# Performance work log

Hardware: AMD Instinct MI355X
Metric: run time of the kernel (lower is better)

## Reference

```python
import jax, jax.numpy as jnp
from jax import lax
import numpy as np

HID = 64      # lstm hidden / gat in-dim
HEADS = 4
DH = HID // HEADS  # 16 per-head dim
OUT = 3       # horizon


def setup_inputs() -> dict:
    key = jax.random.key(0)
    ks = jax.random.split(key, 18)
    B, T, N = 8, 12, 1500
    p = lambda k, shape: jax.random.normal(k, shape, jnp.float32) * 0.1
    return {
        "x": jax.random.normal(ks[0], (B, T, N), jnp.float32),
        "adj": jax.random.randint(ks[1], (N, N), 0, 2, jnp.int32),
        "lstm_Wih0": p(ks[2], (4 * HID, 1)),
        "lstm_Whh0": p(ks[3], (4 * HID, HID)),
        "lstm_bih0": p(ks[4], (4 * HID,)),
        "lstm_bhh0": p(ks[5], (4 * HID,)),
        "lstm_Wih1": p(ks[6], (4 * HID, HID)),
        "lstm_Whh1": p(ks[7], (4 * HID, HID)),
        "lstm_bih1": p(ks[8], (4 * HID,)),
        "lstm_bhh1": p(ks[9], (4 * HID,)),
        "gat0_W": p(ks[10], (HID, HID)),
        "gat0_asrc": p(ks[11], (HEADS, DH)),
        "gat0_adst": p(ks[12], (HEADS, DH)),
        "gat1_W": p(ks[13], (HID, HID)),
        "gat1_asrc": p(ks[14], (HEADS, DH)),
        "gat1_adst": p(ks[15], (HEADS, DH)),
        "out_W": p(ks[16], (OUT, HID)),
        "out_b": p(ks[17], (OUT,)),
    }


def _lstm_layer(seq, Wih, Whh, bih, bhh):
    # seq: (T, BN, in) -> (T, BN, H). PyTorch gate order i,f,g,o.
    BN = seq.shape[1]
    H = Whh.shape[1]

    def step(carry, xt):
        h, c = carry
        g = xt @ Wih.T + h @ Whh.T + bih + bhh
        i, f, gg, o = jnp.split(g, 4, axis=-1)
        c = jax.nn.sigmoid(f) * c + jax.nn.sigmoid(i) * jnp.tanh(gg)
        h = jax.nn.sigmoid(o) * jnp.tanh(c)
        return (h, c), h

    zero = jnp.zeros((BN, H), seq.dtype)
    _, hs = lax.scan(step, (zero, zero), seq)
    return hs


def _gat(h_in, W, asrc, adst, mask):
    # h_in: (B,N,HID); mask: (1,N,N,1) bool
    B, N, _ = h_in.shape
    Hn, D = asrc.shape
    hp = (h_in @ W.T).reshape(B, N, Hn, D)           # (B,N,H,D)
    e_src = jnp.einsum('bnhd,hd->bnh', hp, asrc)
    e_dst = jnp.einsum('bnhd,hd->bnh', hp, adst)
    e = e_src[:, :, None, :] + e_dst[:, None, :, :]   # (B,i,j,H)
    e = jnp.where(e > 0, e, 0.2 * e)                  # LeakyReLU(0.2)
    e = jnp.where(mask, e, -jnp.inf)
    alpha = jax.nn.softmax(e, axis=2)                 # softmax over neighbors j
    ho = jnp.einsum('bijh,bjhd->bihd', alpha, hp)
    return ho.reshape(B, N, Hn * D)


def reference(x, adj, lstm_Wih0, lstm_Whh0, lstm_bih0, lstm_bhh0,
              lstm_Wih1, lstm_Whh1, lstm_bih1, lstm_bhh1,
              gat0_W, gat0_asrc, gat0_adst, gat1_W, gat1_asrc, gat1_adst,
              out_W, out_b):
    B, T, N = x.shape
    # (B,T,N) -> (B*N, T, 1) -> time-major (T, B*N, 1)
    xf = jnp.transpose(x, (0, 2, 1)).reshape(B * N, T, 1)
    seq = jnp.transpose(xf, (1, 0, 2))
    hs = _lstm_layer(seq, lstm_Wih0, lstm_Whh0, lstm_bih0, lstm_bhh0)
    hs = _lstm_layer(hs, lstm_Wih1, lstm_Whh1, lstm_bih1, lstm_bhh1)
    h = hs[-1].reshape(B, N, HID)                     # last-step hidden of top layer
    mask = (adj > 0)[None, :, :, None]
    h = jax.nn.relu(_gat(h, gat0_W, gat0_asrc, gat0_adst, mask))
    h = jax.nn.relu(_gat(h, gat1_W, gat1_asrc, gat1_adst, mask))
    out = h @ out_W.T + out_b                         # (B,N,OUT)
    return jnp.transpose(out, (0, 2, 1))              # (B,OUT,N)
```

## Files before the change

### kernel.cpp

```cpp
#include <hip/hip_runtime.h>
#include <hip/hip_bf16.h>


#define BN 12000
#define NNODE 1500
#define NB 8
#define TT 12
#define NPAD 1536
#define LOG2E 1.44269504f

typedef __bf16 bf16x8 __attribute__((ext_vector_type(8)));
typedef __bf16 bf16x4 __attribute__((ext_vector_type(4)));
typedef float  f32x4  __attribute__((ext_vector_type(4)));

__device__ __forceinline__ float rcpf(float v) { return __builtin_amdgcn_rcpf(v); }
__device__ __forceinline__ float exp2f_(float v) { return __builtin_amdgcn_exp2f(v); }
__device__ __forceinline__ float sigf(float v) { return rcpf(1.f + __expf(-v)); }
__device__ __forceinline__ float tanhf_(float v) {
    return fmaf(2.f, rcpf(1.f + __expf(-2.f * v)), -1.f);
}

__device__ __forceinline__ bf16x8 ldcvt(const float* __restrict__ p) {
    f32x4 a = *(const f32x4*)p;
    f32x4 b = *(const f32x4*)(p + 4);
    bf16x8 r;
    #pragma unroll
    for (int i = 0; i < 4; ++i) { r[i] = (__bf16)a[i]; r[4 + i] = (__bf16)b[i]; }
    return r;
}

__global__ __launch_bounds__(512, 1) void lstm_mask(
    const float* __restrict__ x,
    const float* __restrict__ Wih0, const float* __restrict__ Whh0,
    const float* __restrict__ bih0, const float* __restrict__ bhh0,
    const float* __restrict__ Wih1, const float* __restrict__ Whh1,
    const float* __restrict__ bih1, const float* __restrict__ bhh1,
    const int* __restrict__ adj, unsigned int* __restrict__ mask,
    float* __restrict__ hfin)
{
    if (blockIdx.x >= 750) {
        int wid  = (blockIdx.x - 750) * 8 + (threadIdx.x >> 6);
        int lane = threadIdx.x & 63;
        #pragma unroll 4
        for (int u = 0; u < 16; ++u) {
            int task = wid * 16 + u;
            int i = task / 24, ch = task - i * 24;
            int j = ch * 64 + lane;
            int a = (i < NNODE && j < NNODE) ? adj[i * NNODE + j] : 0;
            unsigned long long m = __ballot(a > 0);
            if (lane == 0 && i < 1504) *(unsigned long long*)&mask[i * 48 + ch * 2] = m;
        }
        return;
    }

    __shared__ __align__(16) __bf16 h0s[16 * 72];
    __shared__ __align__(16) __bf16 h1s[16 * 72];
    __shared__ __align__(16) float  xls[TT * 16];

    int tid  = threadIdx.x;
    int w    = __builtin_amdgcn_readfirstlane(tid >> 6);
    int lane = tid & 63;
    int l15  = lane & 15;
    int qd   = lane >> 4;
    bool lo  = l15 < 8;
    int dloc = l15 & 7;
    int d    = 8 * w + dloc;

    for (int e = tid; e < (16 * 72) / 2; e += 512) ((unsigned int*)h1s)[e] = 0u;
    if (tid < TT * 16) {
        int t = tid >> 4, m = tid & 15;
        int s = blockIdx.x * 16 + m;
        int bb = s / NNODE, nn = s - bb * NNODE;
        xls[tid] = x[bb * (TT * NNODE) + t * NNODE + nn];
    }

    int gA = (lo ? 0 : 64) + d;
    int gB = (lo ? 128 : 192) + d;
    bf16x8 B0A[2], B0B[2], B1A[4], B1B[4];
    #pragma unroll
    for (int kt = 0; kt < 2; ++kt) {
        B0A[kt] = ldcvt(&Whh0[gA * 64 + 32 * kt + 8 * qd]);
        B0B[kt] = ldcvt(&Whh0[gB * 64 + 32 * kt + 8 * qd]);
        B1A[kt] = ldcvt(&Wih1[gA * 64 + 32 * kt + 8 * qd]);
        B1B[kt] = ldcvt(&Wih1[gB * 64 + 32 * kt + 8 * qd]);
        B1A[kt + 2] = ldcvt(&Whh1[gA * 64 + 32 * kt + 8 * qd]);
        B1B[kt + 2] = ldcvt(&Whh1[gB * 64 + 32 * kt + 8 * qd]);
    }
    float b0A = bih0[gA] + bhh0[gA], b0B = bih0[gB] + bhh0[gB];
    float b1A = bih1[gA] + bhh1[gA], b1B = bih1[gB] + bhh1[gB];
    float w0A = Wih0[gA], w0B = Wih0[gB];

    float pwi = Wih0[d],       pbi = bih0[d]       + bhh0[d];
    float pwg = Wih0[128 + d], pbg = bih0[128 + d] + bhh0[128 + d];
    float pwo = Wih0[192 + d], pbo = bih0[192 + d] + bhh0[192 + d];

    float c0[2], c1[2];
    c0[0] = c0[1] = c1[0] = c1[1] = 0.f;

    __syncthreads();

    #pragma unroll
    for (int rl = 0; rl < 2; ++rl) {
        int rr = lo ? rl : 2 + rl;
        int m = 4 * qd + rr;
        float xv = xls[m];
        float gi = fmaf(pwi, xv, pbi);
        float gg = fmaf(pwg, xv, pbg);
        float go = fmaf(pwo, xv, pbo);
        float c = sigf(gi) * tanhf_(gg);
        c0[rl] = c;
        h0s[m * 72 + d] = (__bf16)(sigf(go) * tanhf_(c));
    }
    __syncthreads();

    for (int t = 0; t < TT; ++t) {
        bool last = (t == TT - 1);
        bf16x8 a0[2], a1[2];
        #pragma unroll
        for (int kt = 0; kt < 2; ++kt) {
            a0[kt] = *(bf16x8*)&h0s[l15 * 72 + 32 * kt + 8 * qd];
            a1[kt] = *(bf16x8*)&h1s[l15 * 72 + 32 * kt + 8 * qd];
        }
        f32x4 AA1, AB1, AA0, AB0;
        #pragma unroll
        for (int r = 0; r < 4; ++r) { AA1[r] = b1A; AB1[r] = b1B; }
        if (!last) {
            f32x4 xv = *(f32x4*)&xls[(t + 1) * 16 + 4 * qd];
            #pragma unroll
            for (int r = 0; r < 4; ++r) {
                AA0[r] = fmaf(w0A, xv[r], b0A);
                AB0[r] = fmaf(w0B, xv[r], b0B);
            }
        }
        #pragma unroll
        for (int kt = 0; kt < 2; ++kt) {
            AA1 = __builtin_amdgcn_mfma_f32_16x16x32_bf16(a0[kt], B1A[kt], AA1, 0, 0, 0);
            AB1 = __builtin_amdgcn_mfma_f32_16x16x32_bf16(a0[kt], B1B[kt], AB1, 0, 0, 0);
            AA1 = __builtin_amdgcn_mfma_f32_16x16x32_bf16(a1[kt], B1A[kt + 2], AA1, 0, 0, 0);
            AB1 = __builtin_amdgcn_mfma_f32_16x16x32_bf16(a1[kt], B1B[kt + 2], AB1, 0, 0, 0);
        }
        if (!last) {
            #pragma unroll
            for (int kt = 0; kt < 2; ++kt) {
                AA0 = __builtin_amdgcn_mfma_f32_16x16x32_bf16(a0[kt], B0A[kt], AA0, 0, 0, 0);
                AB0 = __builtin_amdgcn_mfma_f32_16x16x32_bf16(a0[kt], B0B[kt], AB0, 0, 0, 0);
            }
        }
        __syncthreads();

        {
            float shA0 = __shfl_xor(lo ? AA1[2] : AA1[0], 8);
            float shA1 = __shfl_xor(lo ? AA1[3] : AA1[1], 8);
            float shB0 = __shfl_xor(lo ? AB1[2] : AB1[0], 8);
            float shB1 = __shfl_xor(lo ? AB1[3] : AB1[1], 8);
            #pragma unroll
            for (int rl = 0; rl < 2; ++rl) {
                int rr = lo ? rl : 2 + rl;
                float ownA = AA1[rr], ownB = AB1[rr];
                float shA = rl ? shA1 : shA0, shB = rl ? shB1 : shB0;
                float gi = lo ? ownA : shA;
                float gf = lo ? shA : ownA;
                float gg = lo ? ownB : shB;
                float go = lo ? shB : ownB;
                float c = sigf(gf) * c1[rl] + sigf(gi) * tanhf_(gg);
                c1[rl] = c;
                float hv = sigf(go) * tanhf_(c);
                int m = 4 * qd + rr;
                if (!last) h1s[m * 72 + d] = (__bf16)hv;
                else       hfin[(blockIdx.x * 16 + m) * 64 + d] = hv;
            }
        }
        if (!last) {
            float shA0 = __shfl_xor(lo ? AA0[2] : AA0[0], 8);
            float shA1 = __shfl_xor(lo ? AA0[3] : AA0[1], 8);
            float shB0 = __shfl_xor(lo ? AB0[2] : AB0[0], 8);
            float shB1 = __shfl_xor(lo ? AB0[3] : AB0[1], 8);
            #pragma unroll
            for (int rl = 0; rl < 2; ++rl) {
                int rr = lo ? rl : 2 + rl;
                float ownA = AA0[rr], ownB = AB0[rr];
                float shA = rl ? shA1 : shA0, shB = rl ? shB1 : shB0;
                float gi = lo ? ownA : shA;
                float gf = lo ? shA : ownA;
                float gg = lo ? ownB : shB;
                float go = lo ? shB : ownB;
                float c = sigf(gf) * c0[rl] + sigf(gi) * tanhf_(gg);
                c0[rl] = c;
                int m = 4 * qd + rr;
                h0s[m * 72 + d] = (__bf16)(sigf(go) * tanhf_(c));
            }
        }
        __syncthreads();
    }
}

__global__ __launch_bounds__(256) void gat_prep(
    const float* __restrict__ hin, const float* __restrict__ W,
    const float* __restrict__ asrc, const float* __restrict__ adst,
    __bf16* __restrict__ hpT, float* __restrict__ esT, float* __restrict__ edT)
{
    __shared__ __align__(16) __bf16 hp_t[64 * 72];
    __shared__ float avs[128];

    int tid  = threadIdx.x;
    int wv   = tid >> 6;
    int lane = tid & 63;
    int l15  = lane & 15;
    int qd   = lane >> 4;

    if (tid < 64)       avs[tid] = asrc[tid] * LOG2E;
    else if (tid < 128) avs[tid] = adst[tid - 64] * LOG2E;

    int s0 = blockIdx.x * 64;
    int sn = s0 + wv * 16 + l15;
    int snc = min(sn, BN - 1);

    bf16x8 Bf[2];
    #pragma unroll
    for (int kt = 0; kt < 2; ++kt) Bf[kt] = ldcvt(&hin[snc * 64 + kt * 32 + qd * 8]);
    __syncthreads();

    f32x4 acc[4];
    #pragma unroll
    for (int mt = 0; mt < 4; ++mt) {
        int dd = mt * 16 + l15;
        bf16x8 A0 = ldcvt(&W[dd * 64 + qd * 8]);
        bf16x8 A1 = ldcvt(&W[dd * 64 + 32 + qd * 8]);
        f32x4 a = {0.f, 0.f, 0.f, 0.f};
        a = __builtin_amdgcn_mfma_f32_16x16x32_bf16(A0, Bf[0], a, 0, 0, 0);
        a = __builtin_amdgcn_mfma_f32_16x16x32_bf16(A1, Bf[1], a, 0, 0, 0);
        acc[mt] = a;
    }

    #pragma unroll
    for (int mt = 0; mt < 4; ++mt) {
        float ts = 0.f, td = 0.f;
        #pragma unroll
        for (int r = 0; r < 4; ++r) {
            int dd = mt * 16 + qd * 4 + r;
            ts = fmaf(acc[mt][r], avs[dd], ts);
            td = fmaf(acc[mt][r], avs[64 + dd], td);
            hp_t[dd * 72 + wv * 16 + l15] = (__bf16)acc[mt][r];
        }
        ts += __shfl_xor(ts, 16); ts += __shfl_xor(ts, 32);
        td += __shfl_xor(td, 16); td += __shfl_xor(td, 32);
        if (qd == 0 && sn < BN) {
            int b = sn / NNODE, n = sn - b * NNODE;
            esT[(b * 4 + mt) * NPAD + n] = ts;
            edT[(b * 4 + mt) * NPAD + n] = td;
        }
    }
    __syncthreads();

    int dim = tid >> 2, seg = tid & 3;
    int b0 = s0 / NNODE, b1 = (s0 + 63) / NNODE;
    if (b0 == b1 && s0 + 63 < BN) {
        int n0 = s0 - b0 * NNODE;
        bf16x4 v0 = *(bf16x4*)&hp_t[dim * 72 + seg * 16];
        bf16x4 v1 = *(bf16x4*)&hp_t[dim * 72 + seg * 16 + 4];
        bf16x4 v2 = *(bf16x4*)&hp_t[dim * 72 + seg * 16 + 8];
        bf16x4 v3 = *(bf16x4*)&hp_t[dim * 72 + seg * 16 + 12];
        __bf16* dst = &hpT[((b0 << 6) + dim) * NPAD + n0 + seg * 16];
        *(bf16x4*)(dst)      = v0;
        *(bf16x4*)(dst + 4)  = v1;
        *(bf16x4*)(dst + 8)  = v2;
        *(bf16x4*)(dst + 12) = v3;
    } else {
        #pragma unroll
        for (int u = 0; u < 16; ++u) {
            int ss = s0 + seg * 16 + u;
            if (ss < BN) {
                int b = ss / NNODE, n = ss - b * NNODE;
                hpT[((b << 6) + dim) * NPAD + n] = hp_t[dim * 72 + seg * 16 + u];
            }
        }
    }
}

__global__ __launch_bounds__(512) void gat_agg(
    const __bf16* __restrict__ hpT, const float* __restrict__ esT,
    const float* __restrict__ edT, const unsigned int* __restrict__ mask,
    float* __restrict__ hout, const float* __restrict__ oW,
    const float* __restrict__ ob, float* __restrict__ outp, int final)
{
    __shared__ float Ss[8][16];
    __shared__ float hbuf[32 * 72];
    __shared__ float oWs[192];
    __shared__ float obs[3];

    int tid  = threadIdx.x;
    int wv   = tid >> 6;
    int lane = tid & 63;
    int l15  = lane & 15;
    int qd   = lane >> 4;
    int hh   = wv & 3;
    int ig   = wv >> 2;
    int b    = blockIdx.x / 47;
    int i0   = (blockIdx.x % 47) * 32;
    int it   = i0 + ig * 16;

    if (final) {
        if (tid < 192) oWs[tid] = oW[tid];
        if (tid < 3)   obs[tid] = ob[tid];
    }

    const __bf16* Brow = hpT + (((b << 6) + (hh << 4) + l15) * NPAD);
    const float* edrow = edT + (b * 4 + hh) * NPAD;
    const unsigned int* mrow = mask + (it + l15) * 48;
    float esv = esT[(b * 4 + hh) * NPAD + it + l15];

    f32x4 acc = {0.f, 0.f, 0.f, 0.f};
    float S = 0.f;

    for (int jt = 0; jt < 12; ++jt) {
        uint4 mw = *(const uint4*)&mrow[jt * 4];
        #pragma unroll
        for (int kt = 0; kt < 4; ++kt) {
            int jk = jt * 128 + kt * 32 + qd * 8;
            float4 e0 = *(const float4*)&edrow[jk];
            float4 e1 = *(const float4*)&edrow[jk + 4];
            unsigned int mb = ((&mw.x)[kt] >> (qd * 8)) & 0xffu;
            float ej[8] = {e0.x, e0.y, e0.z, e0.w, e1.x, e1.y, e1.z, e1.w};
            bf16x8 A;
            #pragma unroll
            for (int jj = 0; jj < 8; ++jj) {
                float e = esv + ej[jj];
                e = fmaxf(e, 0.2f * e);
                float p = ((mb >> jj) & 1u) ? exp2f_(e) : 0.f;
                S += p;
                A[jj] = (__bf16)p;
            }
            bf16x8 B = *(const bf16x8*)&Brow[jk];
            acc = __builtin_amdgcn_mfma_f32_16x16x32_bf16(A, B, acc, 0, 0, 0);
        }
    }

    S += __shfl_xor(S, 16);
    S += __shfl_xor(S, 32);
    if (qd == 0) Ss[wv][l15] = S;
    __syncthreads();

    if (!final) {
        #pragma unroll
        for (int r = 0; r < 4; ++r) {
            int i = it + qd * 4 + r;
            if (i < NNODE) {
                float rs = rcpf(Ss[wv][qd * 4 + r]);
                hout[((b * NNODE + i) << 6) + (hh << 4) + l15] = fmaxf(acc[r] * rs, 0.f);
            }
        }
    } else {
        #pragma unroll
        for (int r = 0; r < 4; ++r) {
            float rs = rcpf(Ss[wv][qd * 4 + r]);
            hbuf[(ig * 16 + qd * 4 + r) * 72 + (hh << 4) + l15] = fmaxf(acc[r] * rs, 0.f);
        }
        __syncthreads();
        if (tid < 384) {
            int idx = tid >> 2, ks = tid & 3;
            int nl = idx & 31, o = idx >> 5;
            if (i0 + nl < NNODE) {
                const float* hb = &hbuf[nl * 72 + ks * 16];
                float a = 0.f;
                #pragma unroll
                for (int kk = 0; kk < 16; ++kk)
                    a = fmaf(hb[kk], oWs[o * 64 + ks * 16 + kk], a);
                a += __shfl_xor(a, 1);
                a += __shfl_xor(a, 2);
                if (ks == 0)
                    outp[(long)b * 3 * NNODE + o * NNODE + i0 + nl] = a + obs[o];
            }
        }
    }
}

extern "C" void kernel_launch(void* const* d_in, const int* in_sizes, int n_in,
                              void* d_out, int out_size, void* d_ws, size_t ws_size,
                              hipStream_t stream) {
    const float* x    = (const float*)d_in[0];
    const int*   adj  = (const int*)d_in[1];
    const float* Wih0 = (const float*)d_in[2];
    const float* Whh0 = (const float*)d_in[3];
    const float* bih0 = (const float*)d_in[4];
    const float* bhh0 = (const float*)d_in[5];
    const float* Wih1 = (const float*)d_in[6];
    const float* Whh1 = (const float*)d_in[7];
    const float* bih1 = (const float*)d_in[8];
    const float* bhh1 = (const float*)d_in[9];
    const float* g0W  = (const float*)d_in[10];
    const float* g0s  = (const float*)d_in[11];
    const float* g0d  = (const float*)d_in[12];
    const float* g1W  = (const float*)d_in[13];
    const float* g1s  = (const float*)d_in[14];
    const float* g1d  = (const float*)d_in[15];
    const float* oW   = (const float*)d_in[16];
    const float* ob   = (const float*)d_in[17];

    float* ws = (float*)d_ws;
    float*        bufh  = ws;
    float*        esT   = ws + 768000;
    float*        edT   = ws + 817152;
    __bf16*       hpT   = (__bf16*)(ws + 866304);
    unsigned int* maskp = (unsigned int*)(ws + 1259520);

    lstm_mask<<<1032, 512, 0, stream>>>(x, Wih0, Whh0, bih0, bhh0,
                                        Wih1, Whh1, bih1, bhh1,
                                        adj, maskp, bufh);
    gat_prep<<<188, 256, 0, stream>>>(bufh, g0W, g0s, g0d, hpT, esT, edT);
    gat_agg<<<376, 512, 0, stream>>>(hpT, esT, edT, maskp, bufh,
                                     oW, ob, (float*)d_out, 0);
    gat_prep<<<188, 256, 0, stream>>>(bufh, g1W, g1s, g1d, hpT, esT, edT);
    gat_agg<<<376, 512, 0, stream>>>(hpT, esT, edT, maskp, bufh,
                                     oW, ob, (float*)d_out, 1);
}
```

Measured before the change: 231.8 us.

## Fuse GAT projection prep into LSTM and aggregation kernels, cutting launches

Folds the GAT layer-0 projection (h@W, attention logits, transposed bf16 hp) into the tail of the LSTM kernel using the final hidden state already in shared memory. It also folds the layer-1 projection into the layer-0 aggregation epilogue, which becomes gat_mid. This removes two gat_prep launches and the fp32 hidden-state round trip through global memory. Separate buffers for each layer avoid read/write conflicts. In exchange the MFMA projection is now spread over more, smaller blocks, and the LSTM and aggregation blocks do extra tail work.

```diff
diff --git a/kernel.cpp b/kernel.cpp
--- a/kernel.cpp
+++ b/kernel.cpp
@@ -20,7 +20,7 @@
     return fmaf(2.f, rcpf(1.f + __expf(-2.f * v)), -1.f);
 }
 
-__device__ __forceinline__ bf16x8 ldcvt(const float* __restrict__ p) {
+__device__ __forceinline__ bf16x8 ldcvt(const float* p) {
     f32x4 a = *(const f32x4*)p;
     f32x4 b = *(const f32x4*)(p + 4);
     bf16x8 r;
@@ -29,14 +29,16 @@
     return r;
 }
 
-__global__ __launch_bounds__(512, 1) void lstm_mask(
+__global__ __launch_bounds__(512, 1) void lstm_mask_prep(
     const float* __restrict__ x,
     const float* __restrict__ Wih0, const float* __restrict__ Whh0,
     const float* __restrict__ bih0, const float* __restrict__ bhh0,
     const float* __restrict__ Wih1, const float* __restrict__ Whh1,
     const float* __restrict__ bih1, const float* __restrict__ bhh1,
     const int* __restrict__ adj, unsigned int* __restrict__ mask,
-    float* __restrict__ hfin)
+    const float* __restrict__ gW, const float* __restrict__ asrc,
+    const float* __restrict__ adst,
+    __bf16* __restrict__ hpT, float* __restrict__ esT, float* __restrict__ edT)
 {
     if (blockIdx.x >= 750) {
         int wid  = (blockIdx.x - 750) * 8 + (threadIdx.x >> 6);
@@ -56,6 +58,8 @@
     __shared__ __align__(16) __bf16 h0s[16 * 72];
     __shared__ __align__(16) __bf16 h1s[16 * 72];
     __shared__ __align__(16) float  xls[TT * 16];
+    __shared__ float avs[128];
+    __shared__ __align__(16) __bf16 hp_t[64 * 24];
 
     int tid  = threadIdx.x;
     int w    = __builtin_amdgcn_readfirstlane(tid >> 6);
@@ -73,6 +77,8 @@
         int bb = s / NNODE, nn = s - bb * NNODE;
         xls[tid] = x[bb * (TT * NNODE) + t * NNODE + nn];
     }
+    if (tid < 64)       avs[tid] = asrc[tid] * LOG2E;
+    else if (tid < 128) avs[tid] = adst[tid - 64] * LOG2E;
 
     int gA = (lo ? 0 : 64) + d;
     int gB = (lo ? 128 : 192) + d;
@@ -166,8 +172,7 @@
                 c1[rl] = c;
                 float hv = sigf(go) * tanhf_(c);
                 int m = 4 * qd + rr;
-                if (!last) h1s[m * 72 + d] = (__bf16)hv;
-                else       hfin[(blockIdx.x * 16 + m) * 64 + d] = hv;
+                h1s[m * 72 + d] = (__bf16)hv;
             }
         }
         if (!last) {
@@ -192,101 +197,63 @@
         }
         __syncthreads();
     }
-}
-
-__global__ __launch_bounds__(256) void gat_prep(
-    const float* __restrict__ hin, const float* __restrict__ W,
-    const float* __restrict__ asrc, const float* __restrict__ adst,
-    __bf16* __restrict__ hpT, float* __restrict__ esT, float* __restrict__ edT)
-{
-    __shared__ __align__(16) __bf16 hp_t[64 * 72];
-    __shared__ float avs[128];
-
-    int tid  = threadIdx.x;
-    int wv   = tid >> 6;
-    int lane = tid & 63;
-    int l15  = lane & 15;
-    int qd   = lane >> 4;
-
-    if (tid < 64)       avs[tid] = asrc[tid] * LOG2E;
-    else if (tid < 128) avs[tid] = adst[tid - 64] * LOG2E;
-
-    int s0 = blockIdx.x * 64;
-    int sn = s0 + wv * 16 + l15;
-    int snc = min(sn, BN - 1);
-
-    bf16x8 Bf[2];
-    #pragma unroll
-    for (int kt = 0; kt < 2; ++kt) Bf[kt] = ldcvt(&hin[snc * 64 + kt * 32 + qd * 8]);
-    __syncthreads();
-
-    f32x4 acc[4];
-    #pragma unroll
-    for (int mt = 0; mt < 4; ++mt) {
-        int dd = mt * 16 + l15;
-        bf16x8 A0 = ldcvt(&W[dd * 64 + qd * 8]);
-        bf16x8 A1 = ldcvt(&W[dd * 64 + 32 + qd * 8]);
+
+    int s0 = blockIdx.x * 16;
+    if (w < 4) {
+        int mt = w;
+        bf16x8 Bf0 = *(bf16x8*)&h1s[l15 * 72 + 8 * qd];
+        bf16x8 Bf1 = *(bf16x8*)&h1s[l15 * 72 + 32 + 8 * qd];
+        bf16x8 A0 = ldcvt(&gW[(mt * 16 + l15) * 64 + 8 * qd]);
+        bf16x8 A1 = ldcvt(&gW[(mt * 16 + l15) * 64 + 32 + 8 * qd]);
         f32x4 a = {0.f, 0.f, 0.f, 0.f};
-        a = __builtin_amdgcn_mfma_f32_16x16x32_bf16(A0, Bf[0], a, 0, 0, 0);
-        a = __builtin_amdgcn_mfma_f32_16x16x32_bf16(A1, Bf[1], a, 0, 0, 0);
-        acc[mt] = a;
-    }
-
-    #pragma unroll
-    for (int mt = 0; mt < 4; ++mt) {
+        a = __builtin_amdgcn_mfma_f32_16x16x32_bf16(A0, Bf0, a, 0, 0, 0);
+        a = __builtin_amdgcn_mfma_f32_16x16x32_bf16(A1, Bf1, a, 0, 0, 0);
         float ts = 0.f, td = 0.f;
         #pragma unroll
         for (int r = 0; r < 4; ++r) {
             int dd = mt * 16 + qd * 4 + r;
-            ts = fmaf(acc[mt][r], avs[dd], ts);
-            td = fmaf(acc[mt][r], avs[64 + dd], td);
-            hp_t[dd * 72 + wv * 16 + l15] = (__bf16)acc[mt][r];
+            ts = fmaf(a[r], avs[dd], ts);
+            td = fmaf(a[r], avs[64 + dd], td);
+            hp_t[dd * 24 + l15] = (__bf16)a[r];
         }
         ts += __shfl_xor(ts, 16); ts += __shfl_xor(ts, 32);
         td += __shfl_xor(td, 16); td += __shfl_xor(td, 32);
-        if (qd == 0 && sn < BN) {
-            int b = sn / NNODE, n = sn - b * NNODE;
+        if (qd == 0) {
+            int s = s0 + l15, b = s / NNODE, n = s - b * NNODE;
             esT[(b * 4 + mt) * NPAD + n] = ts;
             edT[(b * 4 + mt) * NPAD + n] = td;
         }
     }
     __syncthreads();
-
-    int dim = tid >> 2, seg = tid & 3;
-    int b0 = s0 / NNODE, b1 = (s0 + 63) / NNODE;
-    if (b0 == b1 && s0 + 63 < BN) {
-        int n0 = s0 - b0 * NNODE;
-        bf16x4 v0 = *(bf16x4*)&hp_t[dim * 72 + seg * 16];
-        bf16x4 v1 = *(bf16x4*)&hp_t[dim * 72 + seg * 16 + 4];
-        bf16x4 v2 = *(bf16x4*)&hp_t[dim * 72 + seg * 16 + 8];
-        bf16x4 v3 = *(bf16x4*)&hp_t[dim * 72 + seg * 16 + 12];
-        __bf16* dst = &hpT[((b0 << 6) + dim) * NPAD + n0 + seg * 16];
-        *(bf16x4*)(dst)      = v0;
-        *(bf16x4*)(dst + 4)  = v1;
-        *(bf16x4*)(dst + 8)  = v2;
-        *(bf16x4*)(dst + 12) = v3;
-    } else {
-        #pragma unroll
-        for (int u = 0; u < 16; ++u) {
-            int ss = s0 + seg * 16 + u;
-            if (ss < BN) {
+    if (tid < 256) {
+        int dim = tid >> 2, seg = tid & 3;
+        int b0 = s0 / NNODE, b1 = (s0 + 15) / NNODE;
+        if (b0 == b1) {
+            int n0 = s0 - b0 * NNODE;
+            bf16x4 v = *(bf16x4*)&hp_t[dim * 24 + seg * 4];
+            *(bf16x4*)&hpT[((b0 << 6) + dim) * NPAD + n0 + seg * 4] = v;
+        } else {
+            #pragma unroll
+            for (int u = 0; u < 4; ++u) {
+                int ss = s0 + seg * 4 + u;
                 int b = ss / NNODE, n = ss - b * NNODE;
-                hpT[((b << 6) + dim) * NPAD + n] = hp_t[dim * 72 + seg * 16 + u];
-            }
-        }
-    }
-}
-
-__global__ __launch_bounds__(512) void gat_agg(
+                hpT[((b << 6) + dim) * NPAD + n] = hp_t[dim * 24 + seg * 4 + u];
+            }
+        }
+    }
+}
+
+__global__ __launch_bounds__(512, 1) void gat_mid(
     const __bf16* __restrict__ hpT, const float* __restrict__ esT,
     const float* __restrict__ edT, const unsigned int* __restrict__ mask,
-    float* __restrict__ hout, const float* __restrict__ oW,
-    const float* __restrict__ ob, float* __restrict__ outp, int final)
+    const float* __restrict__ gW, const float* __restrict__ asrc,
+    const float* __restrict__ adst,
+    __bf16* __restrict__ hpT1, float* __restrict__ esT1, float* __restrict__ edT1)
 {
     __shared__ float Ss[8][16];
     __shared__ float hbuf[32 * 72];
-    __shared__ float oWs[192];
-    __shared__ float obs[3];
+    __shared__ float avs[128];
+    __shared__ __align__(16) __bf16 hp1_t[64 * 40];
 
     int tid  = threadIdx.x;
     int wv   = tid >> 6;
@@ -299,10 +266,8 @@
     int i0   = (blockIdx.x % 47) * 32;
     int it   = i0 + ig * 16;
 
-    if (final) {
-        if (tid < 192) oWs[tid] = oW[tid];
-        if (tid < 3)   obs[tid] = ob[tid];
-    }
+    if (tid < 64)       avs[tid] = asrc[tid] * LOG2E;
+    else if (tid < 128) avs[tid] = adst[tid - 64] * LOG2E;
 
     const __bf16* Brow = hpT + (((b << 6) + (hh << 4) + l15) * NPAD);
     const float* edrow = edT + (b * 4 + hh) * NPAD;
@@ -340,36 +305,127 @@
     if (qd == 0) Ss[wv][l15] = S;
     __syncthreads();
 
-    if (!final) {
+    #pragma unroll
+    for (int r = 0; r < 4; ++r) {
+        float rs = rcpf(Ss[wv][qd * 4 + r]);
+        hbuf[(ig * 16 + qd * 4 + r) * 72 + (hh << 4) + l15] = fmaxf(acc[r] * rs, 0.f);
+    }
+    __syncthreads();
+
+    {
+        int mt = hh;
+        bf16x8 Bf0 = ldcvt(&hbuf[(ig * 16 + l15) * 72 + 8 * qd]);
+        bf16x8 Bf1 = ldcvt(&hbuf[(ig * 16 + l15) * 72 + 32 + 8 * qd]);
+        bf16x8 A0 = ldcvt(&gW[(mt * 16 + l15) * 64 + 8 * qd]);
+        bf16x8 A1 = ldcvt(&gW[(mt * 16 + l15) * 64 + 32 + 8 * qd]);
+        f32x4 a = {0.f, 0.f, 0.f, 0.f};
+        a = __builtin_amdgcn_mfma_f32_16x16x32_bf16(A0, Bf0, a, 0, 0, 0);
+        a = __builtin_amdgcn_mfma_f32_16x16x32_bf16(A1, Bf1, a, 0, 0, 0);
+        float ts = 0.f, td = 0.f;
         #pragma unroll
         for (int r = 0; r < 4; ++r) {
-            int i = it + qd * 4 + r;
-            if (i < NNODE) {
-                float rs = rcpf(Ss[wv][qd * 4 + r]);
-                hout[((b * NNODE + i) << 6) + (hh << 4) + l15] = fmaxf(acc[r] * rs, 0.f);
-            }
-        }
-    } else {
-        #pragma unroll
-        for (int r = 0; r < 4; ++r) {
-            float rs = rcpf(Ss[wv][qd * 4 + r]);
-            hbuf[(ig * 16 + qd * 4 + r) * 72 + (hh << 4) + l15] = fmaxf(acc[r] * rs, 0.f);
-        }
-        __syncthreads();
-        if (tid < 384) {
-            int idx = tid >> 2, ks = tid & 3;
-            int nl = idx & 31, o = idx >> 5;
-            if (i0 + nl < NNODE) {
-                const float* hb = &hbuf[nl * 72 + ks * 16];
-                float a = 0.f;
-                #pragma unroll
-                for (int kk = 0; kk < 16; ++kk)
-                    a = fmaf(hb[kk], oWs[o * 64 + ks * 16 + kk], a);
-                a += __shfl_xor(a, 1);
-                a += __shfl_xor(a, 2);
-                if (ks == 0)
-                    outp[(long)b * 3 * NNODE + o * NNODE + i0 + nl] = a + obs[o];
-            }
+            int dd = mt * 16 + qd * 4 + r;
+            ts = fmaf(a[r], avs[dd], ts);
+            td = fmaf(a[r], avs[64 + dd], td);
+            hp1_t[dd * 40 + ig * 16 + l15] = (__bf16)a[r];
+        }
+        ts += __shfl_xor(ts, 16); ts += __shfl_xor(ts, 32);
+        td += __shfl_xor(td, 16); td += __shfl_xor(td, 32);
+        if (qd == 0) {
+            int n = i0 + ig * 16 + l15;
+            esT1[(b * 4 + mt) * NPAD + n] = ts;
+            edT1[(b * 4 + mt) * NPAD + n] = td;
+        }
+    }
+    __syncthreads();
+    if (tid < 256) {
+        int dim = tid >> 2, seg = tid & 3;
+        bf16x8 v = *(bf16x8*)&hp1_t[dim * 40 + seg * 8];
+        *(bf16x8*)&hpT1[((b << 6) + dim) * NPAD + i0 + seg * 8] = v;
+    }
+}
+
+__global__ __launch_bounds__(512, 1) void gat_fin(
+    const __bf16* __restrict__ hpT, const float* __restrict__ esT,
+    const float* __restrict__ edT, const unsigned int* __restrict__ mask,
+    const float* __restrict__ oW, const float* __restrict__ ob,
+    float* __restrict__ outp)
+{
+    __shared__ float Ss[8][16];
+    __shared__ float hbuf[32 * 72];
+    __shared__ float oWs[192];
+    __shared__ float obs[3];
+
+    int tid  = threadIdx.x;
+    int wv   = tid >> 6;
+    int lane = tid & 63;
+    int l15  = lane & 15;
+    int qd   = lane >> 4;
+    int hh   = wv & 3;
+    int ig   = wv >> 2;
+    int b    = blockIdx.x / 47;
+    int i0   = (blockIdx.x % 47) * 32;
+    int it   = i0 + ig * 16;
+
+    if (tid < 192) oWs[tid] = oW[tid];
+    if (tid < 3)   obs[tid] = ob[tid];
+
+    const __bf16* Brow = hpT + (((b << 6) + (hh << 4) + l15) * NPAD);
+    const float* edrow = edT + (b * 4 + hh) * NPAD;
+    const unsigned int* mrow = mask + (it + l15) * 48;
+    float esv = esT[(b * 4 + hh) * NPAD + it + l15];
+
+    f32x4 acc = {0.f, 0.f, 0.f, 0.f};
+    float S = 0.f;
+
+    for (int jt = 0; jt < 12; ++jt) {
+        uint4 mw = *(const uint4*)&mrow[jt * 4];
+        #pragma unroll
+        for (int kt = 0; kt < 4; ++kt) {
+            int jk = jt * 128 + kt * 32 + qd * 8;
+            float4 e0 = *(const float4*)&edrow[jk];
+            float4 e1 = *(const float4*)&edrow[jk + 4];
+            unsigned int mb = ((&mw.x)[kt] >> (qd * 8)) & 0xffu;
+            float ej[8] = {e0.x, e0.y, e0.z, e0.w, e1.x, e1.y, e1.z, e1.w};
+            bf16x8 A;
+            #pragma unroll
+            for (int jj = 0; jj < 8; ++jj) {
+                float e = esv + ej[jj];
+                e = fmaxf(e, 0.2f * e);
+                float p = ((mb >> jj) & 1u) ? exp2f_(e) : 0.f;
+                S += p;
+                A[jj] = (__bf16)p;
+            }
+            bf16x8 B = *(const bf16x8*)&Brow[jk];
+            acc = __builtin_amdgcn_mfma_f32_16x16x32_bf16(A, B, acc, 0, 0, 0);
+        }
+    }
+
+    S += __shfl_xor(S, 16);
+    S += __shfl_xor(S, 32);
+    if (qd == 0) Ss[wv][l15] = S;
+    __syncthreads();
+
+    #pragma unroll
+    for (int r = 0; r < 4; ++r) {
+        float rs = rcpf(Ss[wv][qd * 4 + r]);
+        hbuf[(ig * 16 + qd * 4 + r) * 72 + (hh << 4) + l15] = fmaxf(acc[r] * rs, 0.f);
+    }
+    __syncthreads();
+
+    if (tid < 384) {
+        int idx = tid >> 2, ks = tid & 3;
+        int nl = idx & 31, o = idx >> 5;
+        if (i0 + nl < NNODE) {
+            const float* hb = &hbuf[nl * 72 + ks * 16];
+            float a = 0.f;
+            #pragma unroll
+            for (int kk = 0; kk < 16; ++kk)
+                a = fmaf(hb[kk], oWs[o * 64 + ks * 16 + kk], a);
+            a += __shfl_xor(a, 1);
+            a += __shfl_xor(a, 2);
+            if (ks == 0)
+                outp[(long)b * 3 * NNODE + o * NNODE + i0 + nl] = a + obs[o];
         }
     }
 }
@@ -397,19 +453,20 @@
     const float* ob   = (const float*)d_in[17];
 
     float* ws = (float*)d_ws;
-    float*        bufh  = ws;
-    float*        esT   = ws + 768000;
-    float*        edT   = ws + 817152;
-    __bf16*       hpT   = (__bf16*)(ws + 866304);
-    unsigned int* maskp = (unsigned int*)(ws + 1259520);
-
-    lstm_mask<<<1032, 512, 0, stream>>>(x, Wih0, Whh0, bih0, bhh0,
-                                        Wih1, Whh1, bih1, bhh1,
-                                        adj, maskp, bufh);
-    gat_prep<<<188, 256, 0, stream>>>(bufh, g0W, g0s, g0d, hpT, esT, edT);
-    gat_agg<<<376, 512, 0, stream>>>(hpT, esT, edT, maskp, bufh,
-                                     oW, ob, (float*)d_out, 0);
-    gat_prep<<<188, 256, 0, stream>>>(bufh, g1W, g1s, g1d, hpT, esT, edT);
-    gat_agg<<<376, 512, 0, stream>>>(hpT, esT, edT, maskp, bufh,
-                                     oW, ob, (float*)d_out, 1);
-}
+    float*        esT0  = ws;
+    float*        edT0  = ws + 49152;
+    float*        esT1  = ws + 98304;
+    float*        edT1  = ws + 147456;
+    __bf16*       hpT0  = (__bf16*)(ws + 196608);
+    __bf16*       hpT1  = (__bf16*)(ws + 589824);
+    unsigned int* maskp = (unsigned int*)(ws + 983040);
+
+    lstm_mask_prep<<<1032, 512, 0, stream>>>(x, Wih0, Whh0, bih0, bhh0,
+                                             Wih1, Whh1, bih1, bhh1,
+                                             adj, maskp, g0W, g0s, g0d,
+                                             hpT0, esT0, edT0);
+    gat_mid<<<376, 512, 0, stream>>>(hpT0, esT0, edT0, maskp,
+                                     g1W, g1s, g1d, hpT1, esT1, edT1);
+    gat_fin<<<376, 512, 0, stream>>>(hpT1, esT1, edT1, maskp,
+                                     oW, ob, (float*)d_out);
+}
```

Result: faster. 219.5 us (-5.3%).
